# Kernel tuning notes

Measured on AMD Instinct MI355X. Metric: run time of the kernel, lower is better.

The kernel has to match this reference:

```python
import jax, jax.numpy as jnp
import numpy as np
from jax import lax

EMBED_DIM = 64

def _dwconv(x, w, b):
    # x: [B,H,W,C], w: [3,3,1,C] (HWIO depthwise), b: [C]
    c = x.shape[-1]
    y = lax.conv_general_dilated(
        x, w, window_strides=(1, 1), padding='SAME',
        dimension_numbers=('NHWC', 'HWIO', 'NHWC'),
        feature_group_count=c)
    return y + b

def setup_inputs() -> dict:
    key = jax.random.key(0)
    ks = jax.random.split(key, 8)
    B, H, W, C = 8, 56, 56, 64
    x = jax.random.normal(ks[0], (B, H, W, C), dtype=jnp.float32)
    wq = jax.random.normal(ks[1], (3, 3, 1, C), dtype=jnp.float32) * 0.1
    wk = jax.random.normal(ks[2], (3, 3, 1, C), dtype=jnp.float32) * 0.1
    wv = jax.random.normal(ks[3], (3, 3, 1, C), dtype=jnp.float32) * 0.1
    bq = jnp.zeros((C,), jnp.float32)
    bk = jnp.zeros((C,), jnp.float32)
    bv = jnp.zeros((C,), jnp.float32)
    Wp = jax.random.normal(ks[4], (C, EMBED_DIM), dtype=jnp.float32) * (1.0 / np.sqrt(C))
    bp = jnp.zeros((EMBED_DIM,), jnp.float32)
    return {"x": x, "wq": wq, "bq": bq, "wk": wk, "bk": bk,
            "wv": wv, "bv": bv, "Wp": Wp, "bp": bp}

def reference(x, wq, bq, wk, bk, wv, bv, Wp, bp):
    B, H, W, C = x.shape
    scale = EMBED_DIM ** (-0.5)  # original DIVIDES by this (i.e. multiplies by sqrt(d))
    q = _dwconv(x, wq, bq).reshape(B, H * W, C)
    k = _dwconv(x, wk, bk).reshape(B, H * W, C)
    v = _dwconv(x, wv, bv).reshape(B, H * W, C)
    scores = jnp.einsum('bnc,bmc->bnm', q, k) / scale  # [B, N, N]
    att = jax.nn.softmax(scores, axis=-1)
    ctx = jnp.einsum('bnm,bmc->bnc', att, v).reshape(B, H, W, C)
    return ctx @ Wp + bp
```

## Files before the change

kernel.cpp:

```cpp
#include <hip/hip_runtime.h>
#include <math.h>
#include <stdint.h>

#define B_ 8
#define H_ 56
#define W_ 56
#define C_ 64
#define N_ (H_*W_)
#define KT 32
#define NCH (N_/KT)
#define QTILE 128
#define NTILES 25
#define KSPLIT 4
#define SCALE_LOG2 11.5415603271f

typedef float    f32x16 __attribute__((ext_vector_type(16)));
typedef short    short8 __attribute__((ext_vector_type(8)));
typedef unsigned u32x4  __attribute__((ext_vector_type(4)));

#define GLOBAL_AS __attribute__((address_space(1)))
#define LDS_AS    __attribute__((address_space(3)))

static __device__ __forceinline__ float bf16lo_f(unsigned w) { return __uint_as_float(w << 16); }
static __device__ __forceinline__ float bf16hi_f(unsigned w) { return __uint_as_float(w & 0xFFFF0000u); }
static __device__ __forceinline__ unsigned pack_bf2(float a, float b) {
    unsigned r;
    asm("v_cvt_pk_bf16_f32 %0, %1, %2" : "=v"(r) : "v"(a), "v"(b));
    return r;
}
static __device__ __forceinline__ float exp2_fast(float x) {
    float r;
    asm("v_exp_f32 %0, %1" : "=v"(r) : "v"(x));
    return r;
}
static __device__ __forceinline__ short8 frag_words(unsigned w0, unsigned w1, unsigned w2, unsigned w3) {
    union { u32x4 u; short8 s; } t;
    t.u = (u32x4){w0, w1, w2, w3};
    return t.s;
}
static __device__ __forceinline__ f32x16 MF(short8 a, short8 b, f32x16 c) {
    return __builtin_amdgcn_mfma_f32_32x32x16_bf16(a, b, c, 0, 0, 0);
}
static __device__ __forceinline__ short8 ldsfragK(const uint8_t* base, int row, int q16) {
    const uint4 u = *(const uint4*)(base + row * 256 + ((q16 ^ (row & 15)) * 16));
    union { uint4 a; short8 s; } t; t.a = u; return t.s;
}
static __device__ __forceinline__ short8 ldsfragV(const uint8_t* base, int row, int wd) {
    const uint4 u = *(const uint4*)(base + row * 80 + wd * 16);
    union { uint4 a; short8 s; } t; t.a = u; return t.s;
}

__global__ __launch_bounds__(256)
void dwconv_fused(const float* __restrict__ x,
                  const float* __restrict__ wq, const float* __restrict__ bq,
                  const float* __restrict__ wk, const float* __restrict__ bk,
                  const float* __restrict__ wv, const float* __restrict__ bv,
                  uint8_t* __restrict__ qbuf, uint8_t* __restrict__ kbuf,
                  uint8_t* __restrict__ vtbuf) {
    __shared__ float tq[32][68];
    __shared__ float tk[32][68];

    const int t   = threadIdx.x;
    const int c   = t & 63;
    const int oct = t >> 6;
    const int og  = blockIdx.x * 4 + oct;
    const int b   = og / (N_ / 8);
    const int po  = og % (N_ / 8);
    const int h0  = po / 7;
    const int w0  = (po - h0 * 7) * 8;
    const int n0  = po * 8;

    float q8[8], k8[8], v8[8];
    const float bqc = bq[c], bkc = bk[c], bvc = bv[c];
    #pragma unroll
    for (int i = 0; i < 8; ++i) { q8[i] = bqc; k8[i] = bkc; v8[i] = bvc; }

    #pragma unroll
    for (int dh = 0; dh < 3; ++dh) {
        int hh = h0 + dh - 1;
        if (hh < 0 || hh >= H_) continue;
        float xv[10];
        #pragma unroll
        for (int j = 0; j < 10; ++j) {
            int ww = w0 + j - 1;
            xv[j] = (ww >= 0 && ww < W_) ? x[(((size_t)b * H_ + hh) * W_ + ww) * C_ + c] : 0.f;
        }
        #pragma unroll
        for (int dw = 0; dw < 3; ++dw) {
            float fq = wq[(dh * 3 + dw) * C_ + c];
            float fk = wk[(dh * 3 + dw) * C_ + c];
            float fv = wv[(dh * 3 + dw) * C_ + c];
            #pragma unroll
            for (int i = 0; i < 8; ++i) {
                float xs = xv[i + dw];
                q8[i] = fmaf(xs, fq, q8[i]);
                k8[i] = fmaf(xs, fk, k8[i]);
                v8[i] = fmaf(xs, fv, v8[i]);
            }
        }
    }
    #pragma unroll
    for (int i = 0; i < 8; ++i) q8[i] *= SCALE_LOG2;

    {
        uint4 vh4; unsigned* vh = (unsigned*)&vh4;
        #pragma unroll
        for (int j = 0; j < 4; ++j) vh[j] = pack_bf2(v8[2*j], v8[2*j+1]);
        int ch32 = po >> 2, ko = po & 3;
        *(uint4*)&vtbuf[((size_t)(b * NCH + ch32) * 64 + c) * 64 + ko * 16] = vh4;
    }

    #pragma unroll
    for (int i = 0; i < 8; ++i) { tq[oct * 8 + i][c] = q8[i]; tk[oct * 8 + i][c] = k8[i]; }
    __syncthreads();

    const int g2 = t & 7;
    const int tl = t >> 3;
    float qv[8], kv[8];
    *(float4*)&qv[0] = *(const float4*)&tq[tl][8 * g2];
    *(float4*)&qv[4] = *(const float4*)&tq[tl][8 * g2 + 4];
    *(float4*)&kv[0] = *(const float4*)&tk[tl][8 * g2];
    *(float4*)&kv[4] = *(const float4*)&tk[tl][8 * g2 + 4];

    uint4 qh4, ql4, kh4, kl4;
    unsigned* qh = (unsigned*)&qh4; unsigned* ql = (unsigned*)&ql4;
    unsigned* kh = (unsigned*)&kh4; unsigned* kl = (unsigned*)&kl4;
    #pragma unroll
    for (int j = 0; j < 4; ++j) {
        float a0 = qv[2*j], a1 = qv[2*j+1];
        qh[j] = pack_bf2(a0, a1);
        ql[j] = pack_bf2(a0 - bf16lo_f(qh[j] & 0xFFFFu), a1 - bf16hi_f(qh[j]));
        float k0 = kv[2*j], k1 = kv[2*j+1];
        kh[j] = pack_bf2(k0, k1);
        kl[j] = pack_bf2(k0 - bf16lo_f(kh[j] & 0xFFFFu), k1 - bf16hi_f(kh[j]));
    }
    const int nf = blockIdx.x * 32 + tl;
    size_t rb = (size_t)nf * 256;
    *(uint4*)&qbuf[rb + g2 * 16]                    = qh4;
    *(uint4*)&qbuf[rb + (8 + g2) * 16]              = ql4;
    *(uint4*)&kbuf[rb + ((g2 ^ (nf & 15))) * 16]       = kh4;
    *(uint4*)&kbuf[rb + (((8 + g2) ^ (nf & 15))) * 16] = kl4;
}

__global__ __launch_bounds__(256, 3)
void attn_part(const uint8_t* __restrict__ qbuf, const uint8_t* __restrict__ kbuf,
               const uint8_t* __restrict__ vtbuf,
               float* __restrict__ part, float* __restrict__ ml) {
    __shared__ __align__(16) uint8_t smem[16384 + 10240];

    const int t    = threadIdx.x;
    const int lane = t & 63;
    const int wv_  = t >> 6;
    const int h    = lane >> 5;
    const int l31  = lane & 31;
    const int bx   = blockIdx.x;
    const int b    = bx & 7;
    const int r2   = bx >> 3;
    const int ks   = r2 / NTILES;
    const int tile = r2 % NTILES;
    const int q0   = tile * QTILE;

    const int c_beg = (NCH * ks) / KSPLIT;
    const int c_end = (NCH * (ks + 1)) / KSPLIT;

    const int qu = q0 + wv_ * 32 + l31;
    const int qr = qu < N_ ? qu : N_ - 1;
    const uint8_t* qrp = qbuf + ((size_t)(b * N_ + qr)) * 256;
    short8 qh[4], ql[4];
    #pragma unroll
    for (int s = 0; s < 4; ++s) {
        union { uint4 a; short8 s8; } th, tl_;
        th.a  = *(const uint4*)(qrp + s * 32 + h * 16);
        tl_.a = *(const uint4*)(qrp + 128 + s * 32 + h * 16);
        qh[s] = th.s8; ql[s] = tl_.s8;
    }

    f32x16 ctx0, ctx1;
    #pragma unroll
    for (int i = 0; i < 16; ++i) { ctx0[i] = 0.f; ctx1[i] = 0.f; }
    float mrun = -INFINITY, lrun = 0.f;

    const int slA = t, slB = 256 + t;
    const int vsA = (slA / 5) * 64 + ((slA % 5) == 4 ? 0 : (slA % 5)) * 16;
    const int vsB = (slB / 5) * 64 + ((slB % 5) == 4 ? 0 : (slB % 5)) * 16;

    auto stage = [&](int ch, int pb) {
        const uint8_t* ksrc = kbuf  + ((size_t)(b * N_ + ch * KT)) * 256;
        const uint8_t* vsrc = vtbuf + ((size_t)(b * NCH + ch)) * 4096;
        uint8_t* kd = smem + pb * 8192;
        uint8_t* vd = smem + 16384 + pb * 5120;
        __builtin_amdgcn_global_load_lds((const GLOBAL_AS uint32_t*)(ksrc + t * 16),
                                         (LDS_AS uint32_t*)(kd + t * 16), 16, 0, 0);
        __builtin_amdgcn_global_load_lds((const GLOBAL_AS uint32_t*)(ksrc + t * 16 + 4096),
                                         (LDS_AS uint32_t*)(kd + t * 16 + 4096), 16, 0, 0);
        __builtin_amdgcn_global_load_lds((const GLOBAL_AS uint32_t*)(vsrc + vsA),
                                         (LDS_AS uint32_t*)(vd + slA * 16), 16, 0, 0);
        if (t < 64)
            __builtin_amdgcn_global_load_lds((const GLOBAL_AS uint32_t*)(vsrc + vsB),
                                             (LDS_AS uint32_t*)(vd + slB * 16), 16, 0, 0);
    };

    stage(c_beg, 0);
    __syncthreads();

    for (int ch = c_beg; ch < c_end; ++ch) {
        const int pb = (ch - c_beg) & 1;
        const uint8_t* Kp = smem + pb * 8192;
        const uint8_t* Vp = smem + 16384 + pb * 5120;
        if (ch + 1 < c_end) stage(ch + 1, pb ^ 1);

        f32x16 s0;
        #pragma unroll
        for (int i = 0; i < 16; ++i) s0[i] = 0.f;
        #pragma unroll
        for (int s = 0; s < 4; ++s) {
            short8 kh0 = ldsfragK(Kp, l31, 2 * s + h);
            short8 kl0 = ldsfragK(Kp, l31, 8 + 2 * s + h);
            s0 = MF(kh0, qh[s], s0);
            s0 = MF(kh0, ql[s], s0);
            s0 = MF(kl0, qh[s], s0);
        }

        float mloc = s0[0];
        #pragma unroll
        for (int i = 1; i < 16; ++i) mloc = fmaxf(mloc, s0[i]);
        float mw = fmaxf(mloc, __shfl_xor(mloc, 32));
        if (mw > mrun + 8.f) {
            float fac = exp2_fast(mrun - mw);
            lrun *= fac;
            #pragma unroll
            for (int i = 0; i < 16; ++i) { ctx0[i] *= fac; ctx1[i] *= fac; }
            mrun = mw;
        }
        float p0[16];
        float lsum = 0.f;
        #pragma unroll
        for (int i = 0; i < 16; ++i) { p0[i] = exp2_fast(s0[i] - mrun); lsum += p0[i]; }
        lrun += lsum + __shfl_xor(lsum, 32);

        unsigned hw0[8], lw0[8];
        #pragma unroll
        for (int j = 0; j < 8; ++j) {
            hw0[j] = pack_bf2(p0[2*j], p0[2*j+1]);
            lw0[j] = pack_bf2(p0[2*j]   - bf16lo_f(hw0[j] & 0xFFFFu),
                              p0[2*j+1] - bf16hi_f(hw0[j]));
        }

#define PV_STEP(S) {                                                          \
        const int base = 4 * (S);                                             \
        unsigned a0 = hw0[base], a1 = hw0[base+1], a2 = hw0[base+2], a3 = hw0[base+3]; \
        unsigned c0 = lw0[base], c1 = lw0[base+1], c2 = lw0[base+2], c3 = lw0[base+3]; \
        unsigned sh0 = __shfl_xor(h ? a0 : a2, 32);                           \
        unsigned sh1 = __shfl_xor(h ? a1 : a3, 32);                           \
        unsigned sl0 = __shfl_xor(h ? c0 : c2, 32);                           \
        unsigned sl1 = __shfl_xor(h ? c1 : c3, 32);                           \
        short8 bh = frag_words(h ? sh0 : a0, h ? sh1 : a1,                    \
                               h ? a2 : sh0, h ? a3 : sh1);                   \
        short8 bl = frag_words(h ? sl0 : c0, h ? sl1 : c1,                    \
                               h ? c2 : sl0, h ? c3 : sl1);                   \
        short8 v0f = ldsfragV(Vp, l31,      2 * (S) + h);                     \
        short8 v1f = ldsfragV(Vp, 32 + l31, 2 * (S) + h);                     \
        ctx0 = MF(v0f, bh, ctx0);  ctx1 = MF(v1f, bh, ctx1);                  \
        ctx0 = MF(v0f, bl, ctx0);  ctx1 = MF(v1f, bl, ctx1);                  \
    }
        PV_STEP(0)
        PV_STEP(1)
#undef PV_STEP

        __syncthreads();
    }

    float* pbase = part + (size_t)bx * 8192 + (wv_ * 32 + l31);
    #pragma unroll
    for (int u = 0; u < 4; ++u)
        #pragma unroll
        for (int rr = 0; rr < 4; ++rr) {
            int cc = 8 * u + 4 * h + rr;
            pbase[(size_t)cc * 128]        = ctx0[4*u + rr];
            pbase[(size_t)(cc + 32) * 128] = ctx1[4*u + rr];
        }
    if (h == 0)
        ((float2*)ml)[(size_t)bx * 128 + wv_ * 32 + l31] = make_float2(mrun, lrun);
}

__global__ __launch_bounds__(256)
void combine(const float* __restrict__ part, const float* __restrict__ ml,
             const float* __restrict__ Wp, const float* __restrict__ bp,
             float* __restrict__ out) {
    __shared__ float cm[64][132];
    __shared__ float fac[KSPLIT][128];

    const int bt = blockIdx.x;
    const int b = bt & 7, tile = bt >> 3;
    const int t = threadIdx.x;

    if (t < 128) {
        float m[KSPLIT], l[KSPLIT];
        #pragma unroll
        for (int ks = 0; ks < KSPLIT; ++ks) {
            float2 v = ((const float2*)ml)[((size_t)((ks * NTILES + tile) * 8 + b)) * 128 + t];
            m[ks] = v.x; l[ks] = v.y;
        }
        float M = fmaxf(fmaxf(m[0], m[1]), fmaxf(m[2], m[3]));
        float L = 0.f;
        float f[KSPLIT];
        #pragma unroll
        for (int ks = 0; ks < KSPLIT; ++ks) { f[ks] = exp2f(m[ks] - M); L += l[ks] * f[ks]; }
        float inv = 1.f / L;
        #pragma unroll
        for (int ks = 0; ks < KSPLIT; ++ks) fac[ks][t] = f[ks] * inv;
    }
    __syncthreads();

    {
        const int c = t >> 2, qg = t & 3;
        #pragma unroll
        for (int j = 0; j < 8; ++j) {
            int q = qg * 32 + j * 4;
            float4 acc = make_float4(0.f, 0.f, 0.f, 0.f);
            #pragma unroll
            for (int ks = 0; ks < KSPLIT; ++ks) {
                const float4 p4 = *(const float4*)&part[(((size_t)((ks * NTILES + tile) * 8 + b)) * 64 + c) * 128 + q];
                const float4 f4 = *(const float4*)&fac[ks][q];
                acc.x = fmaf(p4.x, f4.x, acc.x);
                acc.y = fmaf(p4.y, f4.y, acc.y);
                acc.z = fmaf(p4.z, f4.z, acc.z);
                acc.w = fmaf(p4.w, f4.w, acc.w);
            }
            *(float4*)&cm[c][q] = acc;
        }
    }
    __syncthreads();

    {
        const int q = t >> 1, eh = t & 1;
        float4 y[8];
        #pragma unroll
        for (int e = 0; e < 8; ++e) y[e] = *(const float4*)&bp[eh * 32 + e * 4];
        for (int cc = 0; cc < 64; ++cc) {
            float v = cm[cc][q];
            const float4* w4 = (const float4*)&Wp[cc * 64 + eh * 32];
            #pragma unroll
            for (int e = 0; e < 8; ++e) {
                float4 wv4 = w4[e];
                y[e].x = fmaf(v, wv4.x, y[e].x);
                y[e].y = fmaf(v, wv4.y, y[e].y);
                y[e].z = fmaf(v, wv4.z, y[e].z);
                y[e].w = fmaf(v, wv4.w, y[e].w);
            }
        }
        const int n = tile * QTILE + q;
        if (n < N_) {
            float4* op = (float4*)&out[((size_t)b * N_ + n) * 64 + eh * 32];
            #pragma unroll
            for (int e = 0; e < 8; ++e) op[e] = y[e];
        }
    }
}

extern "C" void kernel_launch(void* const* d_in, const int* in_sizes, int n_in,
                              void* d_out, int out_size, void* d_ws, size_t ws_size,
                              hipStream_t stream) {
    const float* x  = (const float*)d_in[0];
    const float* wq = (const float*)d_in[1];
    const float* bq = (const float*)d_in[2];
    const float* wk = (const float*)d_in[3];
    const float* bk = (const float*)d_in[4];
    const float* wv = (const float*)d_in[5];
    const float* bv = (const float*)d_in[6];
    const float* Wp = (const float*)d_in[7];
    const float* bp = (const float*)d_in[8];
    float* out = (float*)d_out;

    const size_t qk_bytes = (size_t)B_ * N_ * 256;
    const size_t vt_bytes = (size_t)B_ * NCH * 64 * 64;
    uint8_t* qbuf  = (uint8_t*)d_ws;
    uint8_t* kbuf  = qbuf + qk_bytes;
    uint8_t* vtbuf = kbuf + qk_bytes;
    float*   partp = (float*)(vtbuf + vt_bytes);
    float*   mlp   = partp + (size_t)800 * 64 * 128;

    dwconv_fused<<<784, 256, 0, stream>>>(x, wq, bq, wk, bk, wv, bv, qbuf, kbuf, vtbuf);
    attn_part<<<8 * NTILES * KSPLIT, 256, 0, stream>>>(qbuf, kbuf, vtbuf, partp, mlp);
    combine<<<8 * NTILES, 256, 0, stream>>>(partp, mlp, Wp, bp, out);
}
```

Measured before the change: 188.6 us.

## Load K/V fragments directly from global memory, double KSPLIT, split combine blocks

Drops the LDS double-buffered staging of K and V in the attention kernel. Each lane now loads its MFMA fragments straight from global memory, which removes the per-chunk __syncthreads and the XOR swizzle of the K layout. KSPLIT goes from 4 to 8 to create more blocks for parallelism, and the combine kernel is split into half-tiles of 64 queries, giving twice as many blocks. The cost is redundant global and L2 traffic for K/V across the wave's query rows, plus larger partial buffers to write and reduce.

```diff
diff --git a/kernel.cpp b/kernel.cpp
--- a/kernel.cpp
+++ b/kernel.cpp
@@ -11,15 +11,12 @@
 #define NCH (N_/KT)
 #define QTILE 128
 #define NTILES 25
-#define KSPLIT 4
+#define KSPLIT 8
 #define SCALE_LOG2 11.5415603271f
 
 typedef float    f32x16 __attribute__((ext_vector_type(16)));
 typedef short    short8 __attribute__((ext_vector_type(8)));
 typedef unsigned u32x4  __attribute__((ext_vector_type(4)));
-
-#define GLOBAL_AS __attribute__((address_space(1)))
-#define LDS_AS    __attribute__((address_space(3)))
 
 static __device__ __forceinline__ float bf16lo_f(unsigned w) { return __uint_as_float(w << 16); }
 static __device__ __forceinline__ float bf16hi_f(unsigned w) { return __uint_as_float(w & 0xFFFF0000u); }
@@ -41,13 +38,10 @@
 static __device__ __forceinline__ f32x16 MF(short8 a, short8 b, f32x16 c) {
     return __builtin_amdgcn_mfma_f32_32x32x16_bf16(a, b, c, 0, 0, 0);
 }
-static __device__ __forceinline__ short8 ldsfragK(const uint8_t* base, int row, int q16) {
-    const uint4 u = *(const uint4*)(base + row * 256 + ((q16 ^ (row & 15)) * 16));
-    union { uint4 a; short8 s; } t; t.a = u; return t.s;
-}
-static __device__ __forceinline__ short8 ldsfragV(const uint8_t* base, int row, int wd) {
-    const uint4 u = *(const uint4*)(base + row * 80 + wd * 16);
-    union { uint4 a; short8 s; } t; t.a = u; return t.s;
+static __device__ __forceinline__ short8 ldf(const uint8_t* p) {
+    union { uint4 a; short8 s; } t;
+    t.a = *(const uint4*)p;
+    return t.s;
 }
 
 __global__ __launch_bounds__(256)
@@ -68,7 +62,6 @@
     const int po  = og % (N_ / 8);
     const int h0  = po / 7;
     const int w0  = (po - h0 * 7) * 8;
-    const int n0  = po * 8;
 
     float q8[8], k8[8], v8[8];
     const float bqc = bq[c], bkc = bk[c], bvc = bv[c];
@@ -136,18 +129,16 @@
     }
     const int nf = blockIdx.x * 32 + tl;
     size_t rb = (size_t)nf * 256;
-    *(uint4*)&qbuf[rb + g2 * 16]                    = qh4;
-    *(uint4*)&qbuf[rb + (8 + g2) * 16]              = ql4;
-    *(uint4*)&kbuf[rb + ((g2 ^ (nf & 15))) * 16]       = kh4;
-    *(uint4*)&kbuf[rb + (((8 + g2) ^ (nf & 15))) * 16] = kl4;
+    *(uint4*)&qbuf[rb + g2 * 16]       = qh4;
+    *(uint4*)&qbuf[rb + (8 + g2) * 16] = ql4;
+    *(uint4*)&kbuf[rb + g2 * 16]       = kh4;
+    *(uint4*)&kbuf[rb + (8 + g2) * 16] = kl4;
 }
 
 __global__ __launch_bounds__(256, 3)
 void attn_part(const uint8_t* __restrict__ qbuf, const uint8_t* __restrict__ kbuf,
                const uint8_t* __restrict__ vtbuf,
                float* __restrict__ part, float* __restrict__ ml) {
-    __shared__ __align__(16) uint8_t smem[16384 + 10240];
-
     const int t    = threadIdx.x;
     const int lane = t & 63;
     const int wv_  = t >> 6;
@@ -169,10 +160,8 @@
     short8 qh[4], ql[4];
     #pragma unroll
     for (int s = 0; s < 4; ++s) {
-        union { uint4 a; short8 s8; } th, tl_;
-        th.a  = *(const uint4*)(qrp + s * 32 + h * 16);
-        tl_.a = *(const uint4*)(qrp + 128 + s * 32 + h * 16);
-        qh[s] = th.s8; ql[s] = tl_.s8;
+        qh[s] = ldf(qrp + s * 32 + h * 16);
+        ql[s] = ldf(qrp + 128 + s * 32 + h * 16);
     }
 
     f32x16 ctx0, ctx1;
@@ -180,46 +169,23 @@
     for (int i = 0; i < 16; ++i) { ctx0[i] = 0.f; ctx1[i] = 0.f; }
     float mrun = -INFINITY, lrun = 0.f;
 
-    const int slA = t, slB = 256 + t;
-    const int vsA = (slA / 5) * 64 + ((slA % 5) == 4 ? 0 : (slA % 5)) * 16;
-    const int vsB = (slB / 5) * 64 + ((slB % 5) == 4 ? 0 : (slB % 5)) * 16;
-
-    auto stage = [&](int ch, int pb) {
-        const uint8_t* ksrc = kbuf  + ((size_t)(b * N_ + ch * KT)) * 256;
-        const uint8_t* vsrc = vtbuf + ((size_t)(b * NCH + ch)) * 4096;
-        uint8_t* kd = smem + pb * 8192;
-        uint8_t* vd = smem + 16384 + pb * 5120;
-        __builtin_amdgcn_global_load_lds((const GLOBAL_AS uint32_t*)(ksrc + t * 16),
-                                         (LDS_AS uint32_t*)(kd + t * 16), 16, 0, 0);
-        __builtin_amdgcn_global_load_lds((const GLOBAL_AS uint32_t*)(ksrc + t * 16 + 4096),
-                                         (LDS_AS uint32_t*)(kd + t * 16 + 4096), 16, 0, 0);
-        __builtin_amdgcn_global_load_lds((const GLOBAL_AS uint32_t*)(vsrc + vsA),
-                                         (LDS_AS uint32_t*)(vd + slA * 16), 16, 0, 0);
-        if (t < 64)
-            __builtin_amdgcn_global_load_lds((const GLOBAL_AS uint32_t*)(vsrc + vsB),
-                                             (LDS_AS uint32_t*)(vd + slB * 16), 16, 0, 0);
-    };
-
-    stage(c_beg, 0);
-    __syncthreads();
-
     for (int ch = c_beg; ch < c_end; ++ch) {
-        const int pb = (ch - c_beg) & 1;
-        const uint8_t* Kp = smem + pb * 8192;
-        const uint8_t* Vp = smem + 16384 + pb * 5120;
-        if (ch + 1 < c_end) stage(ch + 1, pb ^ 1);
+        const uint8_t* krp = kbuf  + ((size_t)(b * N_ + ch * KT + l31)) * 256 + h * 16;
+        const uint8_t* vrp = vtbuf + ((size_t)(b * NCH + ch)) * 4096 + l31 * 64 + h * 16;
+        short8 kh0 = ldf(krp);        short8 kh1 = ldf(krp + 32);
+        short8 kh2 = ldf(krp + 64);   short8 kh3 = ldf(krp + 96);
+        short8 kl0 = ldf(krp + 128);  short8 kl1 = ldf(krp + 160);
+        short8 kl2 = ldf(krp + 192);  short8 kl3 = ldf(krp + 224);
+        short8 va0 = ldf(vrp);        short8 va1 = ldf(vrp + 32);
+        short8 vb0 = ldf(vrp + 2048); short8 vb1 = ldf(vrp + 2048 + 32);
 
         f32x16 s0;
         #pragma unroll
         for (int i = 0; i < 16; ++i) s0[i] = 0.f;
-        #pragma unroll
-        for (int s = 0; s < 4; ++s) {
-            short8 kh0 = ldsfragK(Kp, l31, 2 * s + h);
-            short8 kl0 = ldsfragK(Kp, l31, 8 + 2 * s + h);
-            s0 = MF(kh0, qh[s], s0);
-            s0 = MF(kh0, ql[s], s0);
-            s0 = MF(kl0, qh[s], s0);
-        }
+        s0 = MF(kh0, qh[0], s0); s0 = MF(kh0, ql[0], s0); s0 = MF(kl0, qh[0], s0);
+        s0 = MF(kh1, qh[1], s0); s0 = MF(kh1, ql[1], s0); s0 = MF(kl1, qh[1], s0);
+        s0 = MF(kh2, qh[2], s0); s0 = MF(kh2, ql[2], s0); s0 = MF(kl2, qh[2], s0);
+        s0 = MF(kh3, qh[3], s0); s0 = MF(kh3, ql[3], s0); s0 = MF(kl3, qh[3], s0);
 
         float mloc = s0[0];
         #pragma unroll
@@ -246,7 +212,7 @@
                               p0[2*j+1] - bf16hi_f(hw0[j]));
         }
 
-#define PV_STEP(S) {                                                          \
+#define PV_STEP(S, VA, VB) {                                                  \
         const int base = 4 * (S);                                             \
         unsigned a0 = hw0[base], a1 = hw0[base+1], a2 = hw0[base+2], a3 = hw0[base+3]; \
         unsigned c0 = lw0[base], c1 = lw0[base+1], c2 = lw0[base+2], c3 = lw0[base+3]; \
@@ -258,16 +224,12 @@
                                h ? a2 : sh0, h ? a3 : sh1);                   \
         short8 bl = frag_words(h ? sl0 : c0, h ? sl1 : c1,                    \
                                h ? c2 : sl0, h ? c3 : sl1);                   \
-        short8 v0f = ldsfragV(Vp, l31,      2 * (S) + h);                     \
-        short8 v1f = ldsfragV(Vp, 32 + l31, 2 * (S) + h);                     \
-        ctx0 = MF(v0f, bh, ctx0);  ctx1 = MF(v1f, bh, ctx1);                  \
-        ctx0 = MF(v0f, bl, ctx0);  ctx1 = MF(v1f, bl, ctx1);                  \
-    }
-        PV_STEP(0)
-        PV_STEP(1)
+        ctx0 = MF(VA, bh, ctx0);  ctx1 = MF(VB, bh, ctx1);                    \
+        ctx0 = MF(VA, bl, ctx0);  ctx1 = MF(VB, bl, ctx1);                    \
+    }
+        PV_STEP(0, va0, vb0)
+        PV_STEP(1, va1, vb1)
 #undef PV_STEP
-
-        __syncthreads();
     }
 
     float* pbase = part + (size_t)bx * 8192 + (wv_ * 32 + l31);
@@ -287,25 +249,31 @@
 void combine(const float* __restrict__ part, const float* __restrict__ ml,
              const float* __restrict__ Wp, const float* __restrict__ bp,
              float* __restrict__ out) {
-    __shared__ float cm[64][132];
-    __shared__ float fac[KSPLIT][128];
-
-    const int bt = blockIdx.x;
-    const int b = bt & 7, tile = bt >> 3;
-    const int t = threadIdx.x;
-
-    if (t < 128) {
-        float m[KSPLIT], l[KSPLIT];
+    __shared__ float cm[64][68];
+    __shared__ float fac[KSPLIT][64];
+
+    const int bx   = blockIdx.x;
+    const int b    = bx & 7;
+    const int r2   = bx >> 3;
+    const int tile = r2 >> 1;
+    const int half = r2 & 1;
+    const int qoff = half * 64;
+    const int t    = threadIdx.x;
+
+    if (t < 64) {
+        float m8[KSPLIT], l8[KSPLIT];
         #pragma unroll
         for (int ks = 0; ks < KSPLIT; ++ks) {
-            float2 v = ((const float2*)ml)[((size_t)((ks * NTILES + tile) * 8 + b)) * 128 + t];
-            m[ks] = v.x; l[ks] = v.y;
-        }
-        float M = fmaxf(fmaxf(m[0], m[1]), fmaxf(m[2], m[3]));
+            float2 v = ((const float2*)ml)[((size_t)((ks * NTILES + tile) * 8 + b)) * 128 + qoff + t];
+            m8[ks] = v.x; l8[ks] = v.y;
+        }
+        float M = m8[0];
+        #pragma unroll
+        for (int ks = 1; ks < KSPLIT; ++ks) M = fmaxf(M, m8[ks]);
         float L = 0.f;
         float f[KSPLIT];
         #pragma unroll
-        for (int ks = 0; ks < KSPLIT; ++ks) { f[ks] = exp2f(m[ks] - M); L += l[ks] * f[ks]; }
+        for (int ks = 0; ks < KSPLIT; ++ks) { f[ks] = exp2f(m8[ks] - M); L = fmaf(l8[ks], f[ks], L); }
         float inv = 1.f / L;
         #pragma unroll
         for (int ks = 0; ks < KSPLIT; ++ks) fac[ks][t] = f[ks] * inv;
@@ -315,12 +283,12 @@
     {
         const int c = t >> 2, qg = t & 3;
         #pragma unroll
-        for (int j = 0; j < 8; ++j) {
-            int q = qg * 32 + j * 4;
+        for (int j = 0; j < 4; ++j) {
+            int q = qg * 16 + j * 4;
             float4 acc = make_float4(0.f, 0.f, 0.f, 0.f);
             #pragma unroll
             for (int ks = 0; ks < KSPLIT; ++ks) {
-                const float4 p4 = *(const float4*)&part[(((size_t)((ks * NTILES + tile) * 8 + b)) * 64 + c) * 128 + q];
+                const float4 p4 = *(const float4*)&part[(((size_t)((ks * NTILES + tile) * 8 + b)) * 64 + c) * 128 + qoff + q];
                 const float4 f4 = *(const float4*)&fac[ks][q];
                 acc.x = fmaf(p4.x, f4.x, acc.x);
                 acc.y = fmaf(p4.y, f4.y, acc.y);
@@ -333,15 +301,15 @@
     __syncthreads();
 
     {
-        const int q = t >> 1, eh = t & 1;
-        float4 y[8];
-        #pragma unroll
-        for (int e = 0; e < 8; ++e) y[e] = *(const float4*)&bp[eh * 32 + e * 4];
+        const int q = t >> 2, eq = t & 3;
+        float4 y[4];
+        #pragma unroll
+        for (int e = 0; e < 4; ++e) y[e] = *(const float4*)&bp[eq * 16 + e * 4];
         for (int cc = 0; cc < 64; ++cc) {
             float v = cm[cc][q];
-            const float4* w4 = (const float4*)&Wp[cc * 64 + eh * 32];
-            #pragma unroll
-            for (int e = 0; e < 8; ++e) {
+            const float4* w4 = (const float4*)&Wp[cc * 64 + eq * 16];
+            #pragma unroll
+            for (int e = 0; e < 4; ++e) {
                 float4 wv4 = w4[e];
                 y[e].x = fmaf(v, wv4.x, y[e].x);
                 y[e].y = fmaf(v, wv4.y, y[e].y);
@@ -349,11 +317,11 @@
                 y[e].w = fmaf(v, wv4.w, y[e].w);
             }
         }
-        const int n = tile * QTILE + q;
+        const int n = tile * QTILE + qoff + q;
         if (n < N_) {
-            float4* op = (float4*)&out[((size_t)b * N_ + n) * 64 + eh * 32];
-            #pragma unroll
-            for (int e = 0; e < 8; ++e) op[e] = y[e];
+            float4* op = (float4*)&out[((size_t)b * N_ + n) * 64 + eq * 16];
+            #pragma unroll
+            for (int e = 0; e < 4; ++e) op[e] = y[e];
         }
     }
 }
@@ -378,9 +346,9 @@
     uint8_t* kbuf  = qbuf + qk_bytes;
     uint8_t* vtbuf = kbuf + qk_bytes;
     float*   partp = (float*)(vtbuf + vt_bytes);
-    float*   mlp   = partp + (size_t)800 * 64 * 128;
+    float*   mlp   = partp + (size_t)1600 * 64 * 128;
 
     dwconv_fused<<<784, 256, 0, stream>>>(x, wq, bq, wk, bk, wv, bv, qbuf, kbuf, vtbuf);
     attn_part<<<8 * NTILES * KSPLIT, 256, 0, stream>>>(qbuf, kbuf, vtbuf, partp, mlp);
-    combine<<<8 * NTILES, 256, 0, stream>>>(partp, mlp, Wp, bp, out);
-}
+    combine<<<8 * NTILES * 2, 256, 0, stream>>>(partp, mlp, Wp, bp, out);
+}
```

Result: slower. 231.6 us (+22.8%).

## Double key split, raise attention occupancy, add MFMA priority, split combine blocks

Applied to the files above, without the earlier changes.

Doubles the number of key-range splits in the attention kernel from 4 to 8, giving 1600 blocks instead of 800 so more CUs are busy. The launch-bounds occupancy hint goes from 3 to 6, and s_setprio is raised around the MFMA sections. The combine kernel is split into two half-tile blocks per query tile to match the larger partial count. The cost is twice the partial-result traffic and combine work, plus more register pressure from the higher occupancy target.

```diff
diff --git a/kernel.cpp b/kernel.cpp
--- a/kernel.cpp
+++ b/kernel.cpp
@@ -11,7 +11,7 @@
 #define NCH (N_/KT)
 #define QTILE 128
 #define NTILES 25
-#define KSPLIT 4
+#define KSPLIT 8
 #define SCALE_LOG2 11.5415603271f
 
 typedef float    f32x16 __attribute__((ext_vector_type(16)));
@@ -68,7 +68,6 @@
     const int po  = og % (N_ / 8);
     const int h0  = po / 7;
     const int w0  = (po - h0 * 7) * 8;
-    const int n0  = po * 8;
 
     float q8[8], k8[8], v8[8];
     const float bqc = bq[c], bkc = bk[c], bvc = bv[c];
@@ -142,7 +141,7 @@
     *(uint4*)&kbuf[rb + (((8 + g2) ^ (nf & 15))) * 16] = kl4;
 }
 
-__global__ __launch_bounds__(256, 3)
+__global__ __launch_bounds__(256, 6)
 void attn_part(const uint8_t* __restrict__ qbuf, const uint8_t* __restrict__ kbuf,
                const uint8_t* __restrict__ vtbuf,
                float* __restrict__ part, float* __restrict__ ml) {
@@ -212,6 +211,7 @@
         f32x16 s0;
         #pragma unroll
         for (int i = 0; i < 16; ++i) s0[i] = 0.f;
+        __builtin_amdgcn_s_setprio(1);
         #pragma unroll
         for (int s = 0; s < 4; ++s) {
             short8 kh0 = ldsfragK(Kp, l31, 2 * s + h);
@@ -220,6 +220,7 @@
             s0 = MF(kh0, ql[s], s0);
             s0 = MF(kl0, qh[s], s0);
         }
+        __builtin_amdgcn_s_setprio(0);
 
         float mloc = s0[0];
         #pragma unroll
@@ -246,6 +247,7 @@
                               p0[2*j+1] - bf16hi_f(hw0[j]));
         }
 
+        __builtin_amdgcn_s_setprio(1);
 #define PV_STEP(S) {                                                          \
         const int base = 4 * (S);                                             \
         unsigned a0 = hw0[base], a1 = hw0[base+1], a2 = hw0[base+2], a3 = hw0[base+3]; \
@@ -266,6 +268,7 @@
         PV_STEP(0)
         PV_STEP(1)
 #undef PV_STEP
+        __builtin_amdgcn_s_setprio(0);
 
         __syncthreads();
     }
@@ -287,25 +290,31 @@
 void combine(const float* __restrict__ part, const float* __restrict__ ml,
              const float* __restrict__ Wp, const float* __restrict__ bp,
              float* __restrict__ out) {
-    __shared__ float cm[64][132];
-    __shared__ float fac[KSPLIT][128];
-
-    const int bt = blockIdx.x;
-    const int b = bt & 7, tile = bt >> 3;
-    const int t = threadIdx.x;
-
-    if (t < 128) {
-        float m[KSPLIT], l[KSPLIT];
+    __shared__ float cm[64][68];
+    __shared__ float fac[KSPLIT][64];
+
+    const int bx   = blockIdx.x;
+    const int b    = bx & 7;
+    const int r2   = bx >> 3;
+    const int tile = r2 >> 1;
+    const int half = r2 & 1;
+    const int qoff = half * 64;
+    const int t    = threadIdx.x;
+
+    if (t < 64) {
+        float m8[KSPLIT], l8[KSPLIT];
         #pragma unroll
         for (int ks = 0; ks < KSPLIT; ++ks) {
-            float2 v = ((const float2*)ml)[((size_t)((ks * NTILES + tile) * 8 + b)) * 128 + t];
-            m[ks] = v.x; l[ks] = v.y;
-        }
-        float M = fmaxf(fmaxf(m[0], m[1]), fmaxf(m[2], m[3]));
+            float2 v = ((const float2*)ml)[((size_t)((ks * NTILES + tile) * 8 + b)) * 128 + qoff + t];
+            m8[ks] = v.x; l8[ks] = v.y;
+        }
+        float M = m8[0];
+        #pragma unroll
+        for (int ks = 1; ks < KSPLIT; ++ks) M = fmaxf(M, m8[ks]);
         float L = 0.f;
         float f[KSPLIT];
         #pragma unroll
-        for (int ks = 0; ks < KSPLIT; ++ks) { f[ks] = exp2f(m[ks] - M); L += l[ks] * f[ks]; }
+        for (int ks = 0; ks < KSPLIT; ++ks) { f[ks] = exp2f(m8[ks] - M); L = fmaf(l8[ks], f[ks], L); }
         float inv = 1.f / L;
         #pragma unroll
         for (int ks = 0; ks < KSPLIT; ++ks) fac[ks][t] = f[ks] * inv;
@@ -315,12 +324,12 @@
     {
         const int c = t >> 2, qg = t & 3;
         #pragma unroll
-        for (int j = 0; j < 8; ++j) {
-            int q = qg * 32 + j * 4;
+        for (int j = 0; j < 4; ++j) {
+            int q = qg * 16 + j * 4;
             float4 acc = make_float4(0.f, 0.f, 0.f, 0.f);
             #pragma unroll
             for (int ks = 0; ks < KSPLIT; ++ks) {
-                const float4 p4 = *(const float4*)&part[(((size_t)((ks * NTILES + tile) * 8 + b)) * 64 + c) * 128 + q];
+                const float4 p4 = *(const float4*)&part[(((size_t)((ks * NTILES + tile) * 8 + b)) * 64 + c) * 128 + qoff + q];
                 const float4 f4 = *(const float4*)&fac[ks][q];
                 acc.x = fmaf(p4.x, f4.x, acc.x);
                 acc.y = fmaf(p4.y, f4.y, acc.y);
@@ -333,15 +342,15 @@
     __syncthreads();
 
     {
-        const int q = t >> 1, eh = t & 1;
-        float4 y[8];
-        #pragma unroll
-        for (int e = 0; e < 8; ++e) y[e] = *(const float4*)&bp[eh * 32 + e * 4];
+        const int q = t >> 2, eq = t & 3;
+        float4 y[4];
+        #pragma unroll
+        for (int e = 0; e < 4; ++e) y[e] = *(const float4*)&bp[eq * 16 + e * 4];
         for (int cc = 0; cc < 64; ++cc) {
             float v = cm[cc][q];
-            const float4* w4 = (const float4*)&Wp[cc * 64 + eh * 32];
-            #pragma unroll
-            for (int e = 0; e < 8; ++e) {
+            const float4* w4 = (const float4*)&Wp[cc * 64 + eq * 16];
+            #pragma unroll
+            for (int e = 0; e < 4; ++e) {
                 float4 wv4 = w4[e];
                 y[e].x = fmaf(v, wv4.x, y[e].x);
                 y[e].y = fmaf(v, wv4.y, y[e].y);
@@ -349,11 +358,11 @@
                 y[e].w = fmaf(v, wv4.w, y[e].w);
             }
         }
-        const int n = tile * QTILE + q;
+        const int n = tile * QTILE + qoff + q;
         if (n < N_) {
-            float4* op = (float4*)&out[((size_t)b * N_ + n) * 64 + eh * 32];
-            #pragma unroll
-            for (int e = 0; e < 8; ++e) op[e] = y[e];
+            float4* op = (float4*)&out[((size_t)b * N_ + n) * 64 + eq * 16];
+            #pragma unroll
+            for (int e = 0; e < 4; ++e) op[e] = y[e];
         }
     }
 }
@@ -378,9 +387,9 @@
     uint8_t* kbuf  = qbuf + qk_bytes;
     uint8_t* vtbuf = kbuf + qk_bytes;
     float*   partp = (float*)(vtbuf + vt_bytes);
-    float*   mlp   = partp + (size_t)800 * 64 * 128;
+    float*   mlp   = partp + (size_t)1600 * 64 * 128;
 
     dwconv_fused<<<784, 256, 0, stream>>>(x, wq, bq, wk, bk, wv, bv, qbuf, kbuf, vtbuf);
     attn_part<<<8 * NTILES * KSPLIT, 256, 0, stream>>>(qbuf, kbuf, vtbuf, partp, mlp);
-    combine<<<8 * NTILES, 256, 0, stream>>>(partp, mlp, Wp, bp, out);
-}
+    combine<<<8 * NTILES * 2, 256, 0, stream>>>(partp, mlp, Wp, bp, out);
+}
```

Result: slower. 276.2 us (+46.4%).
